# Performance work log

Hardware: AMD Instinct MI355X
Metric: run time of the kernel (lower is better)

The kernel has to match this reference:

```python
import jax, jax.numpy as jnp
import numpy as np

B, S, E = 2, 2048, 5120
HQ, HKV, HD = 32, 8, 128          # q heads, kv heads, head_dim (hard-coded 128 in source)
DQ, DKV = HQ * HD, HKV * HD       # 4096, 1024
ROPE_THETA = 1.0e9
NEG = -1e30


def setup_inputs() -> dict:
    key = jax.random.key(0)
    k0, k1, k2, k3, k4 = jax.random.split(key, 5)
    x = jax.random.normal(k0, (B, S, E), jnp.float32)
    wq = jax.random.normal(k1, (DQ, E), jnp.float32) * 0.02
    wk = jax.random.normal(k2, (DKV, E), jnp.float32) * 0.02
    wv = jax.random.normal(k3, (DKV, E), jnp.float32) * 0.02
    wo = jax.random.normal(k4, (E, DQ), jnp.float32) * 0.02
    # rotary frequencies: complex freqs_cis[s, HD//2] = exp(i * s * theta^{-2j/HD})
    inv_freq = 1.0 / (ROPE_THETA ** (jnp.arange(0, HD, 2, dtype=jnp.float32) / HD))  # [64]
    ang = jnp.arange(S, dtype=jnp.float32)[:, None] * inv_freq[None, :]              # [S, 64]
    return {
        "x": x,
        "freqs_cos": jnp.cos(ang),
        "freqs_sin": jnp.sin(ang),
        "wq": wq, "wk": wk, "wv": wv, "wo": wo,
    }


def _apply_rope(t, cos, sin):
    # t: [b, s, h, HD//2, 2] viewed as complex pairs; cos/sin: [1, s, 1, HD//2]
    tr, ti = t[..., 0], t[..., 1]
    out = jnp.stack([tr * cos - ti * sin, tr * sin + ti * cos], axis=-1)
    b, s, h = t.shape[0], t.shape[1], t.shape[2]
    return out.reshape(b, s, h, HD)


def reference(x, freqs_cos, freqs_sin, wq, wk, wv, wo):
    b, s, _ = x.shape
    q = (x @ wq.T).reshape(b, s, HQ, HD // 2, 2)
    k = (x @ wk.T).reshape(b, s, HKV, HD // 2, 2)
    v = (x @ wv.T).reshape(b, s, HKV, HD)
    cos = freqs_cos[:s][None, :, None, :]
    sin = freqs_sin[:s][None, :, None, :]
    q = _apply_rope(q, cos, sin)                       # [b, s, HQ, HD]
    k = _apply_rope(k, cos, sin)                       # [b, s, HKV, HD]
    # GQA repeat_kv (repeat_interleave along head dim)
    k = jnp.repeat(k, HQ // HKV, axis=2)               # [b, s, HQ, HD]
    v = jnp.repeat(v, HQ // HKV, axis=2)
    q = q.transpose(0, 2, 1, 3)                        # [b, HQ, s, HD]
    k = k.transpose(0, 2, 1, 3)
    v = v.transpose(0, 2, 1, 3)
    scale = 1.0 / np.sqrt(HD).astype(np.float32)
    scores = jnp.einsum('bhqd,bhkd->bhqk', q, k) * scale
    causal = jnp.tril(jnp.ones((s, s), dtype=bool))
    scores = jnp.where(causal[None, None], scores, NEG)
    attn = jax.nn.softmax(scores, axis=-1)
    out = jnp.einsum('bhqk,bhkd->bhqd', attn, v)       # [b, HQ, s, HD]
    out = out.transpose(0, 2, 1, 3).reshape(b, s, DQ)
    return out @ wo.T                                  # [b, s, E]
```

## Files before the change

### kernel.cpp

```cpp
#include <hip/hip_runtime.h>


typedef unsigned short u16;
typedef __bf16 bf16x8 __attribute__((ext_vector_type(8)));
typedef __bf16 bf16x4 __attribute__((ext_vector_type(4)));
typedef float f32x4 __attribute__((ext_vector_type(4)));

__device__ __forceinline__ u16 f2bf(float f) {
  unsigned u = __builtin_bit_cast(unsigned, f);
  u += 0x7fff + ((u >> 16) & 1);
  return (u16)(u >> 16);
}
__device__ __forceinline__ float bf2f(u16 h) {
  unsigned u = ((unsigned)h) << 16;
  return __builtin_bit_cast(float, u);
}

__device__ __forceinline__ float exp2_hw(float x) {
#if __has_builtin(__builtin_amdgcn_exp2f)
  return __builtin_amdgcn_exp2f(x);
#else
  return __expf(x * 0.6931471805599453f);
#endif
}

__device__ __forceinline__ void gload_lds16(const u16* g, u16* lds) {
  __builtin_amdgcn_global_load_lds(
      (const __attribute__((address_space(1))) void*)g,
      (__attribute__((address_space(3))) void*)lds, 16, 0, 0);
}

__device__ __forceinline__ f32x4 mfma16(bf16x8 a, bf16x8 b, f32x4 c) {
  return __builtin_amdgcn_mfma_f32_16x16x32_bf16(a, b, c, 0, 0, 0);
}

#define VMW(N) asm volatile("s_waitcnt vmcnt(" #N ")" ::: "memory")
#define BAR()  __builtin_amdgcn_s_barrier()

__global__ __launch_bounds__(256) void cvt4_kernel(const float4* __restrict__ s0,
                                                   const float4* __restrict__ s1,
                                                   const float4* __restrict__ s2,
                                                   const float4* __restrict__ s3,
                                                   uint2* __restrict__ d0,
                                                   uint2* __restrict__ d1,
                                                   uint2* __restrict__ d2,
                                                   uint2* __restrict__ d3,
                                                   int n0, int n1, int n2, int n3) {
  int total = n0 + n1 + n2 + n3;
  for (int i = blockIdx.x * blockDim.x + threadIdx.x; i < total;
       i += gridDim.x * blockDim.x) {
    const float4* s; uint2* d; int j = i;
    if (j < n0) { s = s0; d = d0; }
    else if ((j -= n0) < n1) { s = s1; d = d1; }
    else if ((j -= n1) < n2) { s = s2; d = d2; }
    else { j -= n2; s = s3; d = d3; }
    float4 v = s[j];
    d[j] = make_uint2((unsigned)f2bf(v.x) | ((unsigned)f2bf(v.y) << 16),
                      (unsigned)f2bf(v.z) | ((unsigned)f2bf(v.w) << 16));
  }
}

__global__ __launch_bounds__(256) void cvt_kernel(const float4* __restrict__ in,
                                                  uint2* __restrict__ out, int n4) {
  int i = blockIdx.x * blockDim.x + threadIdx.x;
  if (i >= n4) return;
  float4 v = in[i];
  unsigned lo = (unsigned)f2bf(v.x) | ((unsigned)f2bf(v.y) << 16);
  unsigned hi = (unsigned)f2bf(v.z) | ((unsigned)f2bf(v.w) << 16);
  out[i] = make_uint2(lo, hi);
}

__global__ __launch_bounds__(256) void rope_kernel(u16* __restrict__ t,
                                                   const float* __restrict__ fcos,
                                                   const float* __restrict__ fsin,
                                                   int hsh, float scale, int total) {
  int idx = blockIdx.x * blockDim.x + threadIdx.x;
  if (idx >= total) return;
  int j = idx & 63;
  int s = (idx >> (6 + hsh)) & 2047;
  float c = fcos[s * 64 + j], sn = fsin[s * 64 + j];
  unsigned* p = (unsigned*)(t + (size_t)idx * 2);
  unsigned v = *p;
  float tr = bf2f((u16)(v & 0xffffu)), ti = bf2f((u16)(v >> 16));
  float orr = (tr * c - ti * sn) * scale;
  float oi  = (tr * sn + ti * c) * scale;
  *p = (unsigned)f2bf(orr) | ((unsigned)f2bf(oi) << 16);
}

template <int MODE>
__global__ __launch_bounds__(256) void gemm_bt(const u16* __restrict__ A,
                                               const u16* __restrict__ B,
                                               void* __restrict__ Cout,
                                               int M, int N, int K) {
  __shared__ u16 As[8192];
  __shared__ u16 Bs[8192];
  const int tid = threadIdx.x;
  const int lane = tid & 63, wave = tid >> 6;
  const int wm = wave >> 1, wn = wave & 1;
  int gx = gridDim.x, gy = gridDim.y, nwg = gx * gy;
  int orig = blockIdx.y * gx + blockIdx.x;
  int mb, nb;
  if ((gx & 1) == 0 && (gy & 3) == 0 && (nwg & 7) == 0) {
    int x = orig & 7, idx = orig >> 3;
    int hy = gy >> 2, qx = gx >> 1;
    mb = (x >> 1) * hy + (idx % hy);
    nb = (x & 1) * qx + (idx / hy);
  } else {
    mb = orig / gx; nb = orig % gx;
  }
  const int m0 = mb * 128, n0 = nb * 128;
  const int lc = lane & 15, lg = lane >> 4;

  f32x4 acc[4][4] = {};
  const int sr = tid >> 3, sc = tid & 7;

  for (int kt = 0; kt < K; kt += 64) {
    __syncthreads();
#pragma unroll
    for (int q = 0; q < 4; ++q) {
      int r = q * 32 + sr;
      int cc = sc ^ (r & 7);
      gload_lds16(A + (size_t)(m0 + r) * K + kt + cc * 8, &As[q * 2048 + tid * 8]);
      gload_lds16(B + (size_t)(n0 + r) * K + kt + cc * 8, &Bs[q * 2048 + tid * 8]);
    }
    __syncthreads();
#pragma unroll
    for (int ks = 0; ks < 2; ++ks) {
      bf16x8 af[4], bfr[4];
#pragma unroll
      for (int m = 0; m < 4; ++m) {
        int r = wm * 64 + m * 16 + lc;
        int gc = ks * 4 + lg;
        af[m] = *(const bf16x8*)&As[r * 64 + ((gc ^ (r & 7)) * 8)];
      }
#pragma unroll
      for (int n = 0; n < 4; ++n) {
        int r = wn * 64 + n * 16 + lc;
        int gc = ks * 4 + lg;
        bfr[n] = *(const bf16x8*)&Bs[r * 64 + ((gc ^ (r & 7)) * 8)];
      }
#pragma unroll
      for (int m = 0; m < 4; ++m)
#pragma unroll
        for (int n = 0; n < 4; ++n)
          acc[m][n] = mfma16(af[m], bfr[n], acc[m][n]);
    }
  }

#pragma unroll
  for (int m = 0; m < 4; ++m) {
#pragma unroll
    for (int n = 0; n < 4; ++n) {
#pragma unroll
      for (int i = 0; i < 4; ++i) {
        int gm = m0 + wm * 64 + m * 16 + lg * 4 + i;
        int gn = n0 + wn * 64 + n * 16 + lc;
        float v = acc[m][n][i];
        if (MODE == 0) {
          ((u16*)Cout)[(size_t)gm * N + gn] = f2bf(v);
        } else if (MODE == 2) {
          size_t addr = ((size_t)((gm >> 11) * 8 + (gn >> 7)) * 128 + (gn & 127)) * 2048 +
                        (gm & 2047);
          ((u16*)Cout)[addr] = f2bf(v);
        } else {
          if (gn < 1024) {
            ((u16*)Cout)[(size_t)gm * 1024 + gn] = f2bf(v);
          } else {
            int gnv = gn - 1024;
            size_t addr = 4194304ull +
                          ((size_t)((gm >> 11) * 8 + (gnv >> 7)) * 128 + (gnv & 127)) * 2048 +
                          (gm & 2047);
            ((u16*)Cout)[addr] = f2bf(v);
          }
        }
      }
    }
  }
}

template <int OUT_F32>
__global__ __launch_bounds__(512, 2) void gemm256(const u16* __restrict__ A,
                                                  const u16* __restrict__ B,
                                                  void* __restrict__ Cout,
                                                  int M, int N, int K) {
  __shared__ u16 lds[2][2][2][8192];
  __shared__ u16 dummy[4096];
  const int tid = threadIdx.x, lane = tid & 63, wave = tid >> 6;
  const int wm = wave >> 2;
  const int wn = wave & 3;
  const int lc = lane & 15, lg = lane >> 4;
  const int bh = wn >> 1;
  const int bs64 = (wn & 1) * 64;
  const int str = tid >> 3, ssc = tid & 7;

  int gx = gridDim.x, gy = gridDim.y;
  int orig = blockIdx.y * gx + blockIdx.x;
  int mb, nb;
  if ((gx & 3) == 0 && (gy & 1) == 0) {
    int x = orig & 7, idx = orig >> 3;
    int hy = gy >> 1, qx = gx >> 2;
    mb = (x >> 2) * hy + (idx % hy);
    nb = (x & 3) * qx + (idx / hy);
  } else {
    mb = orig / gx; nb = orig % gx;
  }
  const int m0 = mb * 256, n0 = nb * 256;

  auto stageA = [&](int buf, int kcol, int r0, bool real) {
    int r = r0 + str, cc = ssc ^ (r & 7);
    const u16* s = A + (size_t)(m0 + r) * K + kcol + cc * 8;
    u16* d0 = real ? &lds[buf][0][0][r0 * 64] : dummy;
    u16* d1 = real ? &lds[buf][0][1][r0 * 64] : dummy;
    gload_lds16(s, d0 + tid * 8);
    gload_lds16(s + (size_t)128 * K, d1 + tid * 8);
  };
  auto stageB = [&](int buf, int kcol, int half, bool real) {
    int r = str, cc = ssc ^ (r & 7);
    int r2 = 64 + str, cc2 = ssc ^ (r2 & 7);
    const u16* s = B + (size_t)(n0 + half * 128) * K + kcol;
    u16* d0 = real ? &lds[buf][1][half][0] : dummy;
    u16* d1 = real ? &lds[buf][1][half][4096] : dummy;
    gload_lds16(s + (size_t)r * K + cc * 8, d0 + tid * 8);
    gload_lds16(s + (size_t)r2 * K + cc2 * 8, d1 + tid * 8);
  };

  f32x4 acc[8][4] = {};
  bf16x8 af[4][2], bfv[4][2];

  const int nk = K >> 6;
  stageB(0, 0, 0, true);
  stageA(0, 0, 0, true);
  stageB(0, 0, 1, true);
  stageA(0, 0, 64, true);
  stageB(1, 64, 0, true);
  stageA(1, 64, 0, true);
  VMW(6);
  BAR();

  for (int t = 0; t < nk; ++t) {
    const int c = t & 1;
    const int t1 = t + 1, t2 = t + 2;
    const int kc1 = (t1 < nk ? t1 : nk - 1) << 6;
    const int kc2 = (t2 < nk ? t2 : nk - 1) << 6;
    const bool h1 = t1 < nk, h2 = t2 < nk;
    const u16* Ab = &lds[c][0][wm][0];
    const u16* Bb = &lds[c][1][bh][0];

#pragma unroll
    for (int m = 0; m < 4; ++m)
#pragma unroll
      for (int kg = 0; kg < 2; ++kg) {
        int r = m * 16 + lc;
        af[m][kg] = *(const bf16x8*)&Ab[r * 64 + (((kg * 4 + lg) ^ (r & 7)) * 8)];
      }
#pragma unroll
    for (int n = 0; n < 2; ++n)
#pragma unroll
      for (int kg = 0; kg < 2; ++kg) {
        int r = bs64 + n * 16 + lc;
        bfv[n][kg] = *(const bf16x8*)&Bb[r * 64 + (((kg * 4 + lg) ^ (r & 7)) * 8)];
      }
    stageB(t1 & 1, kc1, 1, h1);
    BAR();
    __builtin_amdgcn_s_setprio(1);
#pragma unroll
    for (int m = 0; m < 4; ++m)
#pragma unroll
      for (int n = 0; n < 2; ++n)
#pragma unroll
        for (int kg = 0; kg < 2; ++kg)
          acc[m][n] = mfma16(af[m][kg], bfv[n][kg], acc[m][n]);
    __builtin_amdgcn_s_setprio(0);
    BAR();

#pragma unroll
    for (int n = 2; n < 4; ++n)
#pragma unroll
      for (int kg = 0; kg < 2; ++kg) {
        int r = bs64 + n * 16 + lc;
        bfv[n][kg] = *(const bf16x8*)&Bb[r * 64 + (((kg * 4 + lg) ^ (r & 7)) * 8)];
      }
    stageA(t1 & 1, kc1, 64, h1);
    VMW(6);
    BAR();
    __builtin_amdgcn_s_setprio(1);
#pragma unroll
    for (int m = 0; m < 4; ++m)
#pragma unroll
      for (int n = 2; n < 4; ++n)
#pragma unroll
        for (int kg = 0; kg < 2; ++kg)
          acc[m][n] = mfma16(af[m][kg], bfv[n][kg], acc[m][n]);
    __builtin_amdgcn_s_setprio(0);
    BAR();

#pragma unroll
    for (int m = 0; m < 4; ++m)
#pragma unroll
      for (int kg = 0; kg < 2; ++kg) {
        int r = 64 + m * 16 + lc;
        af[m][kg] = *(const bf16x8*)&Ab[r * 64 + (((kg * 4 + lg) ^ (r & 7)) * 8)];
      }
    stageB(t2 & 1, kc2, 0, h2);
    BAR();
    __builtin_amdgcn_s_setprio(1);
#pragma unroll
    for (int m = 0; m < 4; ++m)
#pragma unroll
      for (int n = 0; n < 2; ++n)
#pragma unroll
        for (int kg = 0; kg < 2; ++kg)
          acc[4 + m][n] = mfma16(af[m][kg], bfv[n][kg], acc[4 + m][n]);
    __builtin_amdgcn_s_setprio(0);
    BAR();

    stageA(t2 & 1, kc2, 0, h2);
    VMW(6);
    BAR();
    __builtin_amdgcn_s_setprio(1);
#pragma unroll
    for (int m = 0; m < 4; ++m)
#pragma unroll
      for (int n = 2; n < 4; ++n)
#pragma unroll
        for (int kg = 0; kg < 2; ++kg)
          acc[4 + m][n] = mfma16(af[m][kg], bfv[n][kg], acc[4 + m][n]);
    __builtin_amdgcn_s_setprio(0);
    BAR();
  }

#pragma unroll
  for (int m = 0; m < 8; ++m) {
#pragma unroll
    for (int n = 0; n < 4; ++n) {
#pragma unroll
      for (int i = 0; i < 4; ++i) {
        int gm = m0 + wm * 128 + m * 16 + lg * 4 + i;
        int gn = n0 + wn * 64 + n * 16 + lc;
        float v = acc[m][n][i];
        if (OUT_F32) ((float*)Cout)[(size_t)gm * N + gn] = v;
        else         ((u16*)Cout)[(size_t)gm * N + gn] = f2bf(v);
      }
    }
  }
}

__global__ __launch_bounds__(512) void attn_kernel(const u16* __restrict__ Q,
                                                   const u16* __restrict__ Kg,
                                                   const u16* __restrict__ VT,
                                                   const float* __restrict__ fcos,
                                                   const float* __restrict__ fsin,
                                                   u16* __restrict__ AO) {
  __shared__ u16 Ks[2][8192];
  __shared__ u16 Vs[2][8192];
  __shared__ u16 P_lds[8][16 * 72];
  const int tid = threadIdx.x, lane = tid & 63, w = tid >> 6;
  const int qt = (int)gridDim.x - 1 - (int)blockIdx.x;
  const int h = blockIdx.y, b = blockIdx.z;
  const int hkv = h >> 2;
  const int q0 = qt * 128;
  const int lc = lane & 15, lg = lane >> 4;

  const float qs = 0.12751743558818574f;
  const int srow = q0 + w * 16 + lc;
  bf16x8 qf[4];
  {
    const size_t qrow = ((size_t)(b * 2048 + srow) * 32 + h) * 128;
#pragma unroll
    for (int ks = 0; ks < 4; ++ks) {
      bf16x8 raw = *(const bf16x8*)&Q[qrow + ks * 32 + lg * 8];
      float4 c4 = *(const float4*)&fcos[srow * 64 + ks * 16 + lg * 4];
      float4 s4 = *(const float4*)&fsin[srow * 64 + ks * 16 + lg * 4];
#pragma unroll
      for (int p = 0; p < 4; ++p) {
        float cc = (&c4.x)[p], ss = (&s4.x)[p];
        float tr = (float)raw[2 * p], ti = (float)raw[2 * p + 1];
        qf[ks][2 * p]     = (__bf16)((tr * cc - ti * ss) * qs);
        qf[ks][2 * p + 1] = (__bf16)((tr * ss + ti * cc) * qs);
      }
    }
  }

  f32x4 o[8] = {};
  f32x4 lsum = {0.f, 0.f, 0.f, 0.f};

  const int nsteps = 2 * qt + 2;
  const size_t kpanel = ((size_t)b * 2048 * 8 + hkv) * 128;
  const size_t vpanel = ((size_t)(b * 8 + hkv) * 128) * 2048;

  auto stage = [&](int buf, int step) {
    const int kv0 = step * 64;
#pragma unroll
    for (int p = 0; p < 2; ++p) {
      int r = p * 32 + (tid >> 4);
      int cc = (tid & 15) ^ (r & 15);
      gload_lds16(Kg + kpanel + (size_t)(kv0 + r) * 1024 + cc * 8,
                  &Ks[buf][p * 4096 + tid * 8]);
    }
#pragma unroll
    for (int p = 0; p < 2; ++p) {
      int r = p * 64 + (tid >> 3);
      int cc = (tid & 7) ^ (r & 7);
      gload_lds16(VT + vpanel + (size_t)r * 2048 + kv0 + cc * 8,
                  &Vs[buf][p * 4096 + tid * 8]);
    }
  };

  stage(0, 0);

  for (int step = 0; step < nsteps; ++step) {
    const int kv0 = step * 64;
    __syncthreads();
    if (step + 1 < nsteps) stage((step + 1) & 1, step + 1);
    const u16* kb = Ks[step & 1];
    const u16* vb = Vs[step & 1];

    f32x4 s[4];
#pragma unroll
    for (int nf = 0; nf < 4; ++nf) s[nf] = f32x4{0.f, 0.f, 0.f, 0.f};
    __builtin_amdgcn_s_setprio(1);
#pragma unroll
    for (int ks = 0; ks < 4; ++ks) {
#pragma unroll
      for (int nf = 0; nf < 4; ++nf) {
        int r = nf * 16 + lc;
        int gc = ks * 4 + lg;
        bf16x8 kf = *(const bf16x8*)&kb[r * 128 + ((gc ^ (r & 15)) * 8)];
        s[nf] = mfma16(kf, qf[ks], s[nf]);
      }
    }
    __builtin_amdgcn_s_setprio(0);

    if (step >= 2 * qt) {
      int q = srow;
#pragma unroll
      for (int nf = 0; nf < 4; ++nf) {
#pragma unroll
        for (int i = 0; i < 4; ++i) {
          int kv = kv0 + nf * 16 + lg * 4 + i;
          if (kv > q) s[nf][i] = -1e30f;
        }
      }
    }

#pragma unroll
    for (int nf = 0; nf < 4; ++nf) {
#pragma unroll
      for (int i = 0; i < 4; ++i) s[nf][i] = exp2_hw(s[nf][i]);
      lsum += s[nf];
      bf16x4 pw = {(__bf16)s[nf][0], (__bf16)s[nf][1], (__bf16)s[nf][2], (__bf16)s[nf][3]};
      *(bf16x4*)&P_lds[w][lc * 72 + nf * 16 + lg * 4] = pw;
    }
    asm volatile("s_waitcnt lgkmcnt(0)" ::: "memory");
    __builtin_amdgcn_sched_barrier(0);

    bf16x8 pa[2];
#pragma unroll
    for (int ksv = 0; ksv < 2; ++ksv)
      pa[ksv] = *(const bf16x8*)&P_lds[w][lc * 72 + ksv * 32 + lg * 8];

    __builtin_amdgcn_s_setprio(1);
#pragma unroll
    for (int nfd = 0; nfd < 8; ++nfd) {
#pragma unroll
      for (int ksv = 0; ksv < 2; ++ksv) {
        int r = nfd * 16 + lc;
        int gc = ksv * 4 + lg;
        bf16x8 vf = *(const bf16x8*)&vb[r * 64 + ((gc ^ (r & 7)) * 8)];
        o[nfd] = mfma16(pa[ksv], vf, o[nfd]);
      }
    }
    __builtin_amdgcn_s_setprio(0);
  }

  float t = lsum[0] + lsum[1] + lsum[2] + lsum[3];
  t += __shfl_xor(t, 16, 64);
  t += __shfl_xor(t, 32, 64);
  float linv[4];
#pragma unroll
  for (int i = 0; i < 4; ++i) linv[i] = 1.0f / __shfl(t, lg * 4 + i, 64);

#pragma unroll
  for (int nfd = 0; nfd < 8; ++nfd)
#pragma unroll
    for (int i = 0; i < 4; ++i) {
      int row = q0 + w * 16 + lg * 4 + i;
      AO[((size_t)(b * 2048 + row) * 32 + h) * 128 + nfd * 16 + lc] =
          f2bf(o[nfd][i] * linv[i]);
    }
}

extern "C" void kernel_launch(void* const* d_in, const int* in_sizes, int n_in,
                              void* d_out, int out_size, void* d_ws, size_t ws_size,
                              hipStream_t stream) {
  const float* x    = (const float*)d_in[0];
  const float* fcos = (const float*)d_in[1];
  const float* fsin = (const float*)d_in[2];
  const float* wq   = (const float*)d_in[3];
  const float* wk   = (const float*)d_in[4];
  const float* wv   = (const float*)d_in[5];
  const float* wo   = (const float*)d_in[6];
  float* out = (float*)d_out;

  char* ws = (char*)d_ws;
  u16* xb  = (u16*)(ws + 0);
  u16* wqb = (u16*)(ws + 41943040ull);
  u16* wkb = (u16*)(ws + 83886080ull);
  u16* wvb = (u16*)(ws + 94371840ull);
  u16* Qb  = (u16*)(ws + 104857600ull);
  u16* Kb  = (u16*)(ws + 138412032ull);
  u16* VTb = (u16*)(ws + 146800640ull);
  u16* AOb = xb;
  u16* wob = wqb;

  cvt4_kernel<<<dim3(2048), dim3(256), 0, stream>>>(
      (const float4*)x, (const float4*)wq, (const float4*)wk, (const float4*)wv,
      (uint2*)xb, (uint2*)wqb, (uint2*)wkb, (uint2*)wvb,
      2 * 2048 * 5120 / 4, 4096 * 5120 / 4, 1024 * 5120 / 4, 1024 * 5120 / 4);

  dim3 blk(256);
  gemm256<0><<<dim3(16, 16), dim3(512), 0, stream>>>(xb, wqb, Qb, 4096, 4096, 5120);
  gemm_bt<3><<<dim3(16, 32), blk, 0, stream>>>(xb, wkb, Kb, 4096, 2048, 5120);

  cvt_kernel<<<dim3(5242880 / 256), blk, 0, stream>>>((const float4*)wo, (uint2*)wob,
                                                      5242880);

  rope_kernel<<<dim3(2097152 / 256), blk, 0, stream>>>(Kb, fcos, fsin, 3, 1.0f, 2097152);

  attn_kernel<<<dim3(16, 32, 2), dim3(512), 0, stream>>>(Qb, Kb, VTb, fcos, fsin, AOb);

  gemm256<1><<<dim3(20, 16), dim3(512), 0, stream>>>(AOb, wob, out, 4096, 5120, 4096);
}
```

Before: 731.6 us.

## Software-pipeline LDS fragment reads one phase ahead of MFMA compute in GEMM

Restructures the GEMM main loop so each phase's LDS-to-register fragment loads for the next MFMA group are issued right after the current MFMA block, inside the same barrier region. A prologue preloads the first A/B fragments, and the next tile's fragments are read from the other LDS buffer at the end of each iteration. The goal is to overlap ds_read latency with MFMA execution and shorten the barrier-separated phases. The vmcnt wait points are moved and changed (VMW(6) and VMW(2)), which carries a risk of data races on the double buffer. Dead helper code (rdA, afv) is left behind.

```diff
diff --git a/kernel.cpp b/kernel.cpp
--- a/kernel.cpp
+++ b/kernel.cpp
@@ -225,7 +225,20 @@
   };
 
   f32x4 acc[8][4] = {};
-  bf16x8 af[4][2], bfv[4][2];
+  bf16x8 afv[4], bfv[4];
+
+  auto rdA = [&](const u16* Ab, int rbase) {
+#pragma unroll
+    for (int m = 0; m < 4; ++m)
+#pragma unroll
+      for (int kg = 0; kg < 2; ++kg) {
+        int r = rbase + m * 16 + lc;
+        (void)r;
+      }
+  };
+  (void)rdA;
+
+  bf16x8 afk[4][2], bfk[4][2];
 
   const int nk = K >> 6;
   stageB(0, 0, 0, true);
@@ -236,6 +249,24 @@
   stageA(1, 64, 0, true);
   VMW(6);
   BAR();
+  {
+    const u16* Ab = &lds[0][0][wm][0];
+    const u16* Bb = &lds[0][1][bh][0];
+#pragma unroll
+    for (int m = 0; m < 4; ++m)
+#pragma unroll
+      for (int kg = 0; kg < 2; ++kg) {
+        int r = m * 16 + lc;
+        afk[m][kg] = *(const bf16x8*)&Ab[r * 64 + (((kg * 4 + lg) ^ (r & 7)) * 8)];
+      }
+#pragma unroll
+    for (int n = 0; n < 2; ++n)
+#pragma unroll
+      for (int kg = 0; kg < 2; ++kg) {
+        int r = bs64 + n * 16 + lc;
+        bfk[n][kg] = *(const bf16x8*)&Bb[r * 64 + (((kg * 4 + lg) ^ (r & 7)) * 8)];
+      }
+  }
 
   for (int t = 0; t < nk; ++t) {
     const int c = t & 1;
@@ -245,87 +276,89 @@
     const bool h1 = t1 < nk, h2 = t2 < nk;
     const u16* Ab = &lds[c][0][wm][0];
     const u16* Bb = &lds[c][1][bh][0];
-
+    const u16* Abn = &lds[c ^ 1][0][wm][0];
+    const u16* Bbn = &lds[c ^ 1][1][bh][0];
+
+    stageB(t1 & 1, kc1, 1, h1);
+    BAR();
+    __builtin_amdgcn_s_setprio(1);
+#pragma unroll
+    for (int m = 0; m < 4; ++m)
+#pragma unroll
+      for (int n = 0; n < 2; ++n)
+#pragma unroll
+        for (int kg = 0; kg < 2; ++kg)
+          acc[m][n] = mfma16(afk[m][kg], bfk[n][kg], acc[m][n]);
+    __builtin_amdgcn_s_setprio(0);
+#pragma unroll
+    for (int n = 2; n < 4; ++n)
+#pragma unroll
+      for (int kg = 0; kg < 2; ++kg) {
+        int r = bs64 + n * 16 + lc;
+        bfk[n][kg] = *(const bf16x8*)&Bb[r * 64 + (((kg * 4 + lg) ^ (r & 7)) * 8)];
+      }
+    BAR();
+
+    VMW(6);
+    stageA(t1 & 1, kc1, 64, h1);
+    BAR();
+    __builtin_amdgcn_s_setprio(1);
+#pragma unroll
+    for (int m = 0; m < 4; ++m)
+#pragma unroll
+      for (int n = 2; n < 4; ++n)
+#pragma unroll
+        for (int kg = 0; kg < 2; ++kg)
+          acc[m][n] = mfma16(afk[m][kg], bfk[n][kg], acc[m][n]);
+    __builtin_amdgcn_s_setprio(0);
+#pragma unroll
+    for (int m = 0; m < 4; ++m)
+#pragma unroll
+      for (int kg = 0; kg < 2; ++kg) {
+        int r = 64 + m * 16 + lc;
+        afk[m][kg] = *(const bf16x8*)&Ab[r * 64 + (((kg * 4 + lg) ^ (r & 7)) * 8)];
+      }
+    BAR();
+
+    VMW(2);
+    stageB(t2 & 1, kc2, 0, h2);
+    BAR();
+    __builtin_amdgcn_s_setprio(1);
+#pragma unroll
+    for (int m = 0; m < 4; ++m)
+#pragma unroll
+      for (int n = 0; n < 2; ++n)
+#pragma unroll
+        for (int kg = 0; kg < 2; ++kg)
+          acc[4 + m][n] = mfma16(afk[m][kg], bfk[n][kg], acc[4 + m][n]);
+    __builtin_amdgcn_s_setprio(0);
+#pragma unroll
+    for (int n = 0; n < 2; ++n)
+#pragma unroll
+      for (int kg = 0; kg < 2; ++kg) {
+        int r = bs64 + n * 16 + lc;
+        bfk[n][kg] = *(const bf16x8*)&Bbn[r * 64 + (((kg * 4 + lg) ^ (r & 7)) * 8)];
+      }
+    BAR();
+
+    stageA(t2 & 1, kc2, 0, h2);
+    BAR();
+    __builtin_amdgcn_s_setprio(1);
+#pragma unroll
+    for (int m = 0; m < 4; ++m)
+#pragma unroll
+      for (int n = 2; n < 4; ++n)
+#pragma unroll
+        for (int kg = 0; kg < 2; ++kg)
+          acc[4 + m][n] = mfma16(afk[m][kg], bfk[n][kg], acc[4 + m][n]);
+    __builtin_amdgcn_s_setprio(0);
 #pragma unroll
     for (int m = 0; m < 4; ++m)
 #pragma unroll
       for (int kg = 0; kg < 2; ++kg) {
         int r = m * 16 + lc;
-        af[m][kg] = *(const bf16x8*)&Ab[r * 64 + (((kg * 4 + lg) ^ (r & 7)) * 8)];
-      }
-#pragma unroll
-    for (int n = 0; n < 2; ++n)
-#pragma unroll
-      for (int kg = 0; kg < 2; ++kg) {
-        int r = bs64 + n * 16 + lc;
-        bfv[n][kg] = *(const bf16x8*)&Bb[r * 64 + (((kg * 4 + lg) ^ (r & 7)) * 8)];
-      }
-    stageB(t1 & 1, kc1, 1, h1);
-    BAR();
-    __builtin_amdgcn_s_setprio(1);
-#pragma unroll
-    for (int m = 0; m < 4; ++m)
-#pragma unroll
-      for (int n = 0; n < 2; ++n)
-#pragma unroll
-        for (int kg = 0; kg < 2; ++kg)
-          acc[m][n] = mfma16(af[m][kg], bfv[n][kg], acc[m][n]);
-    __builtin_amdgcn_s_setprio(0);
-    BAR();
-
-#pragma unroll
-    for (int n = 2; n < 4; ++n)
-#pragma unroll
-      for (int kg = 0; kg < 2; ++kg) {
-        int r = bs64 + n * 16 + lc;
-        bfv[n][kg] = *(const bf16x8*)&Bb[r * 64 + (((kg * 4 + lg) ^ (r & 7)) * 8)];
-      }
-    stageA(t1 & 1, kc1, 64, h1);
-    VMW(6);
-    BAR();
-    __builtin_amdgcn_s_setprio(1);
-#pragma unroll
-    for (int m = 0; m < 4; ++m)
-#pragma unroll
-      for (int n = 2; n < 4; ++n)
-#pragma unroll
-        for (int kg = 0; kg < 2; ++kg)
-          acc[m][n] = mfma16(af[m][kg], bfv[n][kg], acc[m][n]);
-    __builtin_amdgcn_s_setprio(0);
-    BAR();
-
-#pragma unroll
-    for (int m = 0; m < 4; ++m)
-#pragma unroll
-      for (int kg = 0; kg < 2; ++kg) {
-        int r = 64 + m * 16 + lc;
-        af[m][kg] = *(const bf16x8*)&Ab[r * 64 + (((kg * 4 + lg) ^ (r & 7)) * 8)];
-      }
-    stageB(t2 & 1, kc2, 0, h2);
-    BAR();
-    __builtin_amdgcn_s_setprio(1);
-#pragma unroll
-    for (int m = 0; m < 4; ++m)
-#pragma unroll
-      for (int n = 0; n < 2; ++n)
-#pragma unroll
-        for (int kg = 0; kg < 2; ++kg)
-          acc[4 + m][n] = mfma16(af[m][kg], bfv[n][kg], acc[4 + m][n]);
-    __builtin_amdgcn_s_setprio(0);
-    BAR();
-
-    stageA(t2 & 1, kc2, 0, h2);
-    VMW(6);
-    BAR();
-    __builtin_amdgcn_s_setprio(1);
-#pragma unroll
-    for (int m = 0; m < 4; ++m)
-#pragma unroll
-      for (int n = 2; n < 4; ++n)
-#pragma unroll
-        for (int kg = 0; kg < 2; ++kg)
-          acc[4 + m][n] = mfma16(af[m][kg], bfv[n][kg], acc[4 + m][n]);
-    __builtin_amdgcn_s_setprio(0);
+        afk[m][kg] = *(const bf16x8*)&Abn[r * 64 + (((kg * 4 + lg) ^ (r & 7)) * 8)];
+      }
     BAR();
   }
 
```

Result: no change. 724.4 us (-1.0%).
